# Performance work log

Hardware: AMD Instinct MI355X
Metric: run time of the kernel (lower is better)

Reference implementation:

```python
import jax, jax.numpy as jnp
import numpy as np

ALPHA = 0.2      # LeakyReLU negative slope
NEG_INF = -9e15  # mask value from the original code

def setup_inputs() -> dict:
    key = jax.random.key(0)
    k1, k2, k3, k4 = jax.random.split(key, 4)
    B, M, F_IN, F_OUT = 16, 2048, 128, 64
    h = jax.random.normal(k1, (B, M, F_IN), dtype=jnp.float32)
    adj = jax.random.randint(k2, (B, M, M), 0, 2, dtype=jnp.int32)
    W = jax.random.normal(k3, (F_IN, F_OUT), dtype=jnp.float32) * 0.1
    a = jax.random.normal(k4, (2 * F_OUT, 1), dtype=jnp.float32) * 0.1
    return {"h": h, "adj": adj, "W": W, "a": a}

def reference(h, adj, W, a):
    # h: [B,M,Fin], adj: [B,M,M], W: [Fin,E], a: [2E,1]
    Wh = jnp.matmul(h, W)                      # [B,M,E]
    E = Wh.shape[-1]
    a1, a2 = a[:E, 0], a[E:, 0]
    # decompose a^T [Wh_i || Wh_j] = (Wh_i . a1) + (Wh_j . a2)
    f1 = Wh @ a1                               # [B,M] (source/query term)
    f2 = Wh @ a2                               # [B,M] (target/key term)
    e = jax.nn.leaky_relu(f1[:, :, None] + f2[:, None, :], negative_slope=ALPHA)  # [B,M,M]
    scores = jnp.where(adj > 0, e, NEG_INF)
    attn = jax.nn.softmax(scores, axis=-1)     # [B,M,M]  (dropout p=0 / eval mode)
    h_prime = jnp.matmul(attn, Wh)             # [B,M,E]
    return jax.nn.elu(h_prime)                 # concat=True branch
```

## Files before the change

kernel.cpp:

```cpp
#include <hip/hip_runtime.h>


#define M_     2048
#define FIN_   128
#define F_     64
#define ALPHA_ 0.2f
#define HS_    132
#define WT_    132

typedef float  float4_ __attribute__((ext_vector_type(4)));
typedef short  short8  __attribute__((ext_vector_type(8)));
typedef int    int4_   __attribute__((ext_vector_type(4)));
typedef unsigned int u32x4 __attribute__((ext_vector_type(4)));
typedef unsigned short u16;
typedef unsigned int   u32;

static __device__ __forceinline__ u32 cvtpk(float lo, float hi) {
    u32 r;
    asm("v_cvt_pk_bf16_f32 %0, %1, %2" : "=v"(r) : "v"(lo), "v"(hi));
    return r;
}

__global__ __launch_bounds__(256, 4) void k_prep(
    const float* __restrict__ h, const float* __restrict__ W,
    const float* __restrict__ a, u16* __restrict__ hbf,
    float* __restrict__ f1all, float* __restrict__ f2all)
{
    __shared__ float a_s[2 * F_];
    __shared__ float wa1[FIN_], wa2[FIN_];
    __shared__ float hs[32 * HS_];

    const int tid = threadIdx.x;
    const u32 bid = blockIdx.x;
    const u32 lg  = (bid & 7) * 128 + (bid >> 3);
    const int b   = lg >> 6;
    const int t   = lg & 63;

    if (tid < 128) a_s[tid] = a[tid];

    const int tok = tid >> 3, f0 = (tid & 7) * 16;
    const float* hp = h + ((size_t)(b * M_ + t * 32 + tok)) * FIN_ + f0;
    float4_ x0 = *(const float4_*)hp;
    float4_ x1 = *(const float4_*)(hp + 4);
    float4_ x2 = *(const float4_*)(hp + 8);
    float4_ x3 = *(const float4_*)(hp + 12);
    __syncthreads();

    if (tid < FIN_) {
        float s1 = 0.f, s2 = 0.f;
#pragma unroll 8
        for (int n = 0; n < F_; ++n) {
            float wv = W[tid * F_ + n];
            s1 += wv * a_s[n];
            s2 += wv * a_s[F_ + n];
        }
        wa1[tid] = s1;
        wa2[tid] = s2;
    }

    float* hr = hs + tok * HS_ + f0;
    *(float4_*)(hr)      = x0;
    *(float4_*)(hr + 4)  = x1;
    *(float4_*)(hr + 8)  = x2;
    *(float4_*)(hr + 12) = x3;
    __syncthreads();

    {
        const int l = tid & 63, lc = l & 15, q = l >> 4;
        const int nt0 = (tid >> 6) * 2;
        u32x4* ob = (u32x4*)hbf + ((size_t)(b * 64 + t)) * 8 * 64;
#pragma unroll
        for (int ni = 0; ni < 2; ++ni) {
            const int nt = nt0 + ni;
            const float* cp = hs + (q * 8) * HS_ + nt * 16 + lc;
            u32x4 wv;
            wv[0] = cvtpk(cp[0 * HS_], cp[1 * HS_]);
            wv[1] = cvtpk(cp[2 * HS_], cp[3 * HS_]);
            wv[2] = cvtpk(cp[4 * HS_], cp[5 * HS_]);
            wv[3] = cvtpk(cp[6 * HS_], cp[7 * HS_]);
            ob[nt * 64 + l] = wv;
        }
    }

    {
        const int r = tid >> 3, k0 = (tid & 7) * 16;
        const float* rp = hs + r * HS_ + k0;
        float s1 = 0.f, s2 = 0.f;
#pragma unroll
        for (int k = 0; k < 16; ++k) {
            s1 += rp[k] * wa1[k0 + k];
            s2 += rp[k] * wa2[k0 + k];
        }
        s1 += __shfl_xor(s1, 1, 64); s2 += __shfl_xor(s2, 1, 64);
        s1 += __shfl_xor(s1, 2, 64); s2 += __shfl_xor(s2, 2, 64);
        s1 += __shfl_xor(s1, 4, 64); s2 += __shfl_xor(s2, 4, 64);
        if ((tid & 7) == 0) {
            f1all[b * M_ + t * 32 + r] = s1;
            f2all[b * M_ + t * 32 + r] = s2;
        }
    }
}

__global__ __launch_bounds__(128, 4) void k_main(
    const int* __restrict__ adj, const u16* __restrict__ hbf,
    const float* __restrict__ f1all, const float* __restrict__ f2all,
    const float* __restrict__ W, float* __restrict__ out)
{
    __shared__ char  dyn[WT_ * 32 * 4];
    __shared__ float dens[32];

    float* f2s  = (float*)dyn;
    float* Tsum = (float*)dyn;

    const int tid  = threadIdx.x;
    const int w    = tid >> 6;
    const int l    = tid & 63;
    const int lc   = l & 15;
    const int quad = l >> 4;

    const u32 bid = blockIdx.x;
    const u32 lg  = (bid & 7) * 128 + (bid >> 3);
    const int b   = lg >> 6;
    const int i0  = (lg & 63) * 32;
    const int rowbase = i0 + w * 16;

    {
        const int o = tid * 16;
        float4_ v0 = *(const float4_*)(f2all + b * M_ + o);
        float4_ v1 = *(const float4_*)(f2all + b * M_ + o + 4);
        float4_ v2 = *(const float4_*)(f2all + b * M_ + o + 8);
        float4_ v3 = *(const float4_*)(f2all + b * M_ + o + 12);
        *(float4_*)(f2s + o)      = v0;
        *(float4_*)(f2s + o + 4)  = v1;
        *(float4_*)(f2s + o + 8)  = v2;
        *(float4_*)(f2s + o + 12) = v3;
    }

    const float f1r = f1all[b * M_ + rowbase + lc];
    const int* aprow = adj + ((size_t)(b * M_ + rowbase + lc)) * M_ + quad * 8;
    const u32x4* hb  = (const u32x4*)hbf + ((size_t)b * 64) * 8 * 64 + l;

    int4_ aA0 = *(const int4_*)(aprow);
    int4_ aA1 = *(const int4_*)(aprow + 4);
    int4_ aB0 = *(const int4_*)(aprow + 32);
    int4_ aB1 = *(const int4_*)(aprow + 36);
    int4_ aC0 = *(const int4_*)(aprow + 64);
    int4_ aC1 = *(const int4_*)(aprow + 68);

    __syncthreads();

    float denacc = 0.f;
    float4_ acc[8];
#pragma unroll
    for (int nt = 0; nt < 8; ++nt) acc[nt] = (float4_){0.f, 0.f, 0.f, 0.f};

#pragma unroll 2
    for (int t = 0; t < 64; ++t) {
        const int jp = (t < 61 ? t + 3 : 63) * 32;

        int4_ nA0 = *(const int4_*)(aprow + jp);
        int4_ nA1 = *(const int4_*)(aprow + jp + 4);
        u32x4 bb[8];
#pragma unroll
        for (int nt = 0; nt < 8; ++nt) bb[nt] = hb[(t * 8 + nt) * 64];

        float4_ g0 = *(const float4_*)(f2s + t * 32 + quad * 8);
        float4_ g1 = *(const float4_*)(f2s + t * 32 + quad * 8 + 4);

        u32x4 pw;
        float d = 0.f;
#define SC(GE, GO, AE, AO, IDX)                                 \
        {                                                       \
            float xe = f1r + (GE); xe = fmaxf(xe, ALPHA_ * xe); \
            float xo = f1r + (GO); xo = fmaxf(xo, ALPHA_ * xo); \
            float ee = ((AE) > 0) ? __expf(xe) : 0.f;           \
            float eo = ((AO) > 0) ? __expf(xo) : 0.f;           \
            u32 pk = cvtpk(ee, eo);                             \
            d += __uint_as_float(pk << 16);                     \
            d += __uint_as_float(pk & 0xFFFF0000u);             \
            pw[IDX] = pk;                                       \
        }
        SC(g0[0], g0[1], aA0[0], aA0[1], 0)
        SC(g0[2], g0[3], aA0[2], aA0[3], 1)
        SC(g1[0], g1[1], aA1[0], aA1[1], 2)
        SC(g1[2], g1[3], aA1[2], aA1[3], 3)
#undef SC
        denacc += d;
        const short8 af = __builtin_bit_cast(short8, pw);

#pragma unroll
        for (int nt = 0; nt < 8; ++nt)
            acc[nt] = __builtin_amdgcn_mfma_f32_16x16x32_bf16(
                af, __builtin_bit_cast(short8, bb[nt]), acc[nt], 0, 0, 0);

        aA0 = aB0; aA1 = aB1; aB0 = aC0; aB1 = aC1; aC0 = nA0; aC1 = nA1;
    }

    denacc += __shfl_xor(denacc, 16, 64);
    denacc += __shfl_xor(denacc, 32, 64);
    if (quad == 0) dens[w * 16 + lc] = denacc;
    __syncthreads();

#pragma unroll
    for (int nt = 0; nt < 8; ++nt)
#pragma unroll
        for (int mm = 0; mm < 4; ++mm)
            Tsum[(w * 16 + quad * 4 + mm) * WT_ + nt * 16 + lc] = acc[nt][mm];
    __syncthreads();

#pragma unroll
    for (int rr = 0; rr < 2; ++rr) {
        const int r  = (tid >> 3) + rr * 16;
        const int n0 = (tid & 7) * 8;
        const float den  = dens[r];
        const float rden = (den > 0.f) ? (1.f / den) : 0.f;
        float u[8];
#pragma unroll
        for (int nn = 0; nn < 8; ++nn) u[nn] = 0.f;
#pragma unroll 4
        for (int k = 0; k < FIN_; ++k) {
            const float tv = Tsum[r * WT_ + k];
            float4_ wv0 = *(const float4_*)(W + k * F_ + n0);
            float4_ wv1 = *(const float4_*)(W + k * F_ + n0 + 4);
            u[0] += tv * wv0[0]; u[1] += tv * wv0[1];
            u[2] += tv * wv0[2]; u[3] += tv * wv0[3];
            u[4] += tv * wv1[0]; u[5] += tv * wv1[1];
            u[6] += tv * wv1[2]; u[7] += tv * wv1[3];
        }
        float4_ o0, o1;
#pragma unroll
        for (int nn = 0; nn < 8; ++nn) {
            float hp = u[nn] * rden;
            float o  = hp > 0.f ? hp : expm1f(hp);
            if (nn < 4) o0[nn] = o; else o1[nn - 4] = o;
        }
        float* op = out + ((size_t)(b * M_ + i0 + r)) * F_ + n0;
        *(float4_*)op       = o0;
        *(float4_*)(op + 4) = o1;
    }
}

extern "C" void kernel_launch(void* const* d_in, const int* in_sizes, int n_in,
                              void* d_out, int out_size, void* d_ws, size_t ws_size,
                              hipStream_t stream)
{
    (void)out_size; (void)ws_size;
    const float* h  = (const float*)d_in[0];
    const int* adjp = (const int*)d_in[1];
    const float* Wp = (const float*)d_in[2];
    const float* ap = (const float*)d_in[3];
    for (int i = 0; i < n_in; ++i) {
        long s = in_sizes[i];
        if      (s == 4194304L)  h    = (const float*)d_in[i];
        else if (s == 67108864L) adjp = (const int*)d_in[i];
        else if (s == 8192L)     Wp   = (const float*)d_in[i];
        else if (s == 128L)      ap   = (const float*)d_in[i];
    }
    u16*   hbf   = (u16*)d_ws;
    float* f1all = (float*)((char*)d_ws + (8u << 20));
    float* f2all = f1all + 16 * M_;
    k_prep<<<1024, 256, 0, stream>>>(h, Wp, ap, hbf, f1all, f2all);
    k_main<<<1024, 128, 0, stream>>>(adjp, hbf, f1all, f2all, Wp, (float*)d_out);
}
```

Baseline: 435.9 us.

## Double-buffer hbf B-operand loads and deepen adjacency prefetch to four stages

The main loop now prefetches the next tile's bf16 Wh fragments into a ping-pong register buffer while the current tile's MFMAs run. The adjacency prefetch ring grows from three to four stages, held in a register array indexed statically through a 4x manual unroll. Launch bounds drop from 4 to 3 waves-per-EU minimum to make room for the extra registers. The aim is to hide global-load latency behind compute, at the cost of higher register pressure and possibly lower occupancy.

```diff
diff --git a/kernel.cpp b/kernel.cpp
--- a/kernel.cpp
+++ b/kernel.cpp
@@ -101,7 +101,7 @@
     }
 }
 
-__global__ __launch_bounds__(128, 4) void k_main(
+__global__ __launch_bounds__(128, 3) void k_main(
     const int* __restrict__ adj, const u16* __restrict__ hbf,
     const float* __restrict__ f1all, const float* __restrict__ f2all,
     const float* __restrict__ W, float* __restrict__ out)
@@ -140,12 +140,15 @@
     const int* aprow = adj + ((size_t)(b * M_ + rowbase + lc)) * M_ + quad * 8;
     const u32x4* hb  = (const u32x4*)hbf + ((size_t)b * 64) * 8 * 64 + l;
 
-    int4_ aA0 = *(const int4_*)(aprow);
-    int4_ aA1 = *(const int4_*)(aprow + 4);
-    int4_ aB0 = *(const int4_*)(aprow + 32);
-    int4_ aB1 = *(const int4_*)(aprow + 36);
-    int4_ aC0 = *(const int4_*)(aprow + 64);
-    int4_ aC1 = *(const int4_*)(aprow + 68);
+    int4_ aP0[4], aP1[4];
+#pragma unroll
+    for (int i = 0; i < 4; ++i) {
+        aP0[i] = *(const int4_*)(aprow + i * 32);
+        aP1[i] = *(const int4_*)(aprow + i * 32 + 4);
+    }
+    u32x4 bbA[8], bbB[8];
+#pragma unroll
+    for (int nt = 0; nt < 8; ++nt) bbA[nt] = hb[nt * 64];
 
     __syncthreads();
 
@@ -154,21 +157,6 @@
 #pragma unroll
     for (int nt = 0; nt < 8; ++nt) acc[nt] = (float4_){0.f, 0.f, 0.f, 0.f};
 
-#pragma unroll 2
-    for (int t = 0; t < 64; ++t) {
-        const int jp = (t < 61 ? t + 3 : 63) * 32;
-
-        int4_ nA0 = *(const int4_*)(aprow + jp);
-        int4_ nA1 = *(const int4_*)(aprow + jp + 4);
-        u32x4 bb[8];
-#pragma unroll
-        for (int nt = 0; nt < 8; ++nt) bb[nt] = hb[(t * 8 + nt) * 64];
-
-        float4_ g0 = *(const float4_*)(f2s + t * 32 + quad * 8);
-        float4_ g1 = *(const float4_*)(f2s + t * 32 + quad * 8 + 4);
-
-        u32x4 pw;
-        float d = 0.f;
 #define SC(GE, GO, AE, AO, IDX)                                 \
         {                                                       \
             float xe = f1r + (GE); xe = fmaxf(xe, ALPHA_ * xe); \
@@ -180,21 +168,40 @@
             d += __uint_as_float(pk & 0xFFFF0000u);             \
             pw[IDX] = pk;                                       \
         }
-        SC(g0[0], g0[1], aA0[0], aA0[1], 0)
-        SC(g0[2], g0[3], aA0[2], aA0[3], 1)
-        SC(g1[0], g1[1], aA1[0], aA1[1], 2)
-        SC(g1[2], g1[3], aA1[2], aA1[3], 3)
+
+#define STAGE(T, I, BC, BN)                                                   \
+    {                                                                         \
+        const int tn = ((T) < 63) ? (T) + 1 : 63;                             \
+        const int tp = ((T) < 60) ? (T) + 4 : 63;                             \
+        _Pragma("unroll")                                                     \
+        for (int nt = 0; nt < 8; ++nt) BN[nt] = hb[(tn * 8 + nt) * 64];       \
+        float4_ g0 = *(const float4_*)(f2s + (T) * 32 + quad * 8);            \
+        float4_ g1 = *(const float4_*)(f2s + (T) * 32 + quad * 8 + 4);        \
+        u32x4 pw;                                                             \
+        float d = 0.f;                                                        \
+        SC(g0[0], g0[1], aP0[I][0], aP0[I][1], 0)                             \
+        SC(g0[2], g0[3], aP0[I][2], aP0[I][3], 1)                             \
+        SC(g1[0], g1[1], aP1[I][0], aP1[I][1], 2)                             \
+        SC(g1[2], g1[3], aP1[I][2], aP1[I][3], 3)                             \
+        denacc += d;                                                          \
+        const short8 af = __builtin_bit_cast(short8, pw);                     \
+        aP0[I] = *(const int4_*)(aprow + tp * 32);                            \
+        aP1[I] = *(const int4_*)(aprow + tp * 32 + 4);                        \
+        _Pragma("unroll")                                                     \
+        for (int nt = 0; nt < 8; ++nt)                                        \
+            acc[nt] = __builtin_amdgcn_mfma_f32_16x16x32_bf16(                \
+                af, __builtin_bit_cast(short8, BC[nt]), acc[nt], 0, 0, 0);    \
+    }
+
+    for (int o = 0; o < 16; ++o) {
+        const int t0 = o * 4;
+        STAGE(t0 + 0, 0, bbA, bbB)
+        STAGE(t0 + 1, 1, bbB, bbA)
+        STAGE(t0 + 2, 2, bbA, bbB)
+        STAGE(t0 + 3, 3, bbB, bbA)
+    }
+#undef STAGE
 #undef SC
-        denacc += d;
-        const short8 af = __builtin_bit_cast(short8, pw);
-
-#pragma unroll
-        for (int nt = 0; nt < 8; ++nt)
-            acc[nt] = __builtin_amdgcn_mfma_f32_16x16x32_bf16(
-                af, __builtin_bit_cast(short8, bb[nt]), acc[nt], 0, 0, 0);
-
-        aA0 = aB0; aA1 = aB1; aB0 = aC0; aB1 = aC1; aC0 = nA0; aC1 = nA1;
-    }
 
     denacc += __shfl_xor(denacc, 16, 64);
     denacc += __shfl_xor(denacc, 32, 64);
```

Result: slower. 448.0 us (+2.8%).
